# Kernel tuning notes

Hardware: AMD Instinct MI355X
Metric: run time of the kernel (lower is better)

The kernel has to match this reference:

```python
import jax, jax.numpy as jnp
import numpy as np

ALPHA = 0.5
BETA = 0.5
N_CLASS = 128
EPS = 1e-9


def setup_inputs() -> dict:
    key = jax.random.key(0)
    k1, k2 = jax.random.split(key)
    y_pred = jax.random.normal(k1, (262144, N_CLASS), dtype=jnp.float32)
    y_true = jax.random.randint(k2, (262144,), 0, N_CLASS, dtype=jnp.int64)
    return {"y_pred": y_pred, "y_true": y_true}


def reference(y_pred, y_true):
    N = y_pred.shape[0]
    # Cross-entropy (mean reduction, as nn.CrossEntropyLoss default)
    logp = jax.nn.log_softmax(y_pred, axis=1)
    ce = -jnp.mean(jnp.take_along_axis(logp, y_true[:, None], axis=1))

    # Penalty term uses detached probabilities (y_pred.detach() in torch)
    p = jax.nn.softmax(jax.lax.stop_gradient(y_pred), axis=1)
    p1 = p[:, 0]  # probability of class 0 per sample

    # num_labels: class histogram (torch loop -> vectorized scatter-add)
    num_labels = jnp.zeros((N_CLASS,), dtype=y_pred.dtype).at[y_true].add(1.0)
    # sj(j) = beta * (1 - n_j / (sum(n) - n_0)), defined for j >= 1
    s = BETA * (1.0 - num_labels / (jnp.sum(num_labels) - num_labels[0]))

    # per-sample penalty: alpha*log(p1+eps) if label==0 else s[label]*log(1-p1+eps)
    per_sample = jnp.where(
        y_true == 0,
        ALPHA * jnp.log(p1 + EPS),
        s[y_true] * jnp.log(1.0 - p1 + EPS),
    )
    penalty = jnp.sum(per_sample)
    return ce - penalty / N
```

## Files before the change

kernel.cpp:

```cpp
#include <hip/hip_runtime.h>
#include <math.h>
#include <stdint.h>

#define NCLS 128
#define NBANK 8
constexpr float ALPHA = 0.5f;
constexpr float BETA_ = 0.5f;
constexpr float EPS_ = 1e-9f;

__global__ void zero_ws(uint32_t* __restrict__ ws) {
    const int t = threadIdx.x;
    for (int i = t; i < 3088; i += 256) ws[i] = 0u;
}

__global__ __launch_bounds__(1024, 4) void loss_main(
    const float* __restrict__ y_pred,
    const int*   __restrict__ y_true,
    double* __restrict__ gLb, unsigned int* __restrict__ gcntb,
    double* __restrict__ gceb, int nrows)
{
    __shared__ float    sL[NCLS];
    __shared__ unsigned scnt[NCLS];
    __shared__ float    sce;

    const int t = threadIdx.x;
    if (t == 0) sce = 0.f;
    if (t < NCLS) { sL[t] = 0.f; scnt[t] = 0u; }
    __syncthreads();

    const int lane = t & 63;
    const int half = lane >> 5;
    const int l32  = lane & 31;
    const int wgl  = blockIdx.x * (blockDim.x >> 6) + (t >> 6);
    const int nW   = gridDim.x * (blockDim.x >> 6);
    const int nPairs = nrows >> 1;

    float ce_local = 0.f;

    int p0 = wgl * 8;
    for (; p0 + 7 < nPairs; p0 += nW * 8) {
        float4 v[8]; int lab[8];
        const float* base = y_pred + ((size_t)(p0 << 1) + half) * NCLS + (l32 << 2);
        #pragma unroll
        for (int u = 0; u < 8; ++u) {
            v[u]   = *reinterpret_cast<const float4*>(base + (size_t)(u << 1) * NCLS);
            lab[u] = y_true[((p0 + u) << 1) + half];
        }
        __builtin_amdgcn_sched_barrier(0);

        float S[8], e0[8];
        #pragma unroll
        for (int u = 0; u < 8; ++u) {
            const float ex = __expf(v[u].x), ey = __expf(v[u].y);
            const float ez = __expf(v[u].z), ew = __expf(v[u].w);
            e0[u] = ex;
            S[u]  = (ex + ey) + (ez + ew);
            if ((lab[u] >> 2) == l32) {
                const int ls = lab[u] & 3;
                ce_local += (ls == 0) ? v[u].x : (ls == 1) ? v[u].y
                          : (ls == 2) ? v[u].z : v[u].w;
            }
        }
        #pragma unroll
        for (int off = 16; off; off >>= 1) {
            #pragma unroll
            for (int u = 0; u < 8; ++u) S[u] += __shfl_xor(S[u], off);
        }
        float e0m = 1.f, Sm = 1.f; int labm = 0;
        #pragma unroll
        for (int u = 0; u < 8; ++u) {
            const float b = __shfl(e0[u], half << 5);
            if (l32 == u) { e0m = b; Sm = S[u]; labm = lab[u]; }
        }
        if (l32 < 8) {
            const float logS = __logf(Sm);
            ce_local -= logS;
            const float d = (labm == 0) ? e0m : (Sm - e0m);
            const float c0 = __logf(__fmaf_rn(EPS_, Sm, d)) - logS;
            const float contrib = (labm == 0) ? ALPHA * c0 : c0;
            atomicAdd(&sL[labm], contrib);
            atomicAdd(&scnt[labm], 1u);
        }
    }
    for (; p0 < nPairs; ++p0) {
        const int row = (p0 << 1) + half;
        const float4 v = *reinterpret_cast<const float4*>(
            y_pred + (size_t)row * NCLS + (l32 << 2));
        const int lab = y_true[row];
        const float ex = __expf(v.x), ey = __expf(v.y);
        const float ez = __expf(v.z), ew = __expf(v.w);
        float S = (ex + ey) + (ez + ew);
        if ((lab >> 2) == l32) {
            const int ls = lab & 3;
            ce_local += (ls == 0) ? v.x : (ls == 1) ? v.y : (ls == 2) ? v.z : v.w;
        }
        #pragma unroll
        for (int off = 16; off; off >>= 1) S += __shfl_xor(S, off);
        if (l32 == 0) {
            const float logS = __logf(S);
            ce_local -= logS;
            const float d = (lab == 0) ? ex : (S - ex);
            const float c0 = __logf(__fmaf_rn(EPS_, S, d)) - logS;
            const float contrib = (lab == 0) ? ALPHA * c0 : c0;
            atomicAdd(&sL[lab], contrib);
            atomicAdd(&scnt[lab], 1u);
        }
    }
    if ((nrows & 1) && wgl == 0) {
        const int row = nrows - 1;
        const float4 v = *reinterpret_cast<const float4*>(
            y_pred + (size_t)row * NCLS + (l32 << 2));
        const int lab = y_true[row];
        if (half == 0) {
            const float ex = __expf(v.x), ey = __expf(v.y);
            const float ez = __expf(v.z), ew = __expf(v.w);
            float S = (ex + ey) + (ez + ew);
            if ((lab >> 2) == l32) {
                const int ls = lab & 3;
                ce_local += (ls == 0) ? v.x : (ls == 1) ? v.y : (ls == 2) ? v.z : v.w;
            }
            #pragma unroll
            for (int off = 16; off; off >>= 1) S += __shfl_xor(S, off);
            if (l32 == 0) {
                const float logS = __logf(S);
                ce_local -= logS;
                const float d = (lab == 0) ? ex : (S - ex);
                const float c0 = __logf(__fmaf_rn(EPS_, S, d)) - logS;
                const float contrib = (lab == 0) ? ALPHA * c0 : c0;
                atomicAdd(&sL[lab], contrib);
                atomicAdd(&scnt[lab], 1u);
            }
        }
    }

    float lp = ce_local;
    #pragma unroll
    for (int off = 32; off; off >>= 1) lp += __shfl_xor(lp, off);
    if (lane == 0) atomicAdd(&sce, lp);
    __syncthreads();

    const int bank = blockIdx.x & (NBANK - 1);
    if (t < NCLS) {
        const int c = (t + blockIdx.x) & (NCLS - 1);
        if (scnt[c]) {
            atomicAdd(&gLb[c * NBANK + bank], (double)sL[c]);
            atomicAdd(&gcntb[c * NBANK + bank], scnt[c]);
        }
    }
    if (t == 0) atomicAdd(&gceb[bank], (double)sce);
}

__global__ void loss_final(const double* __restrict__ gLb,
                           const unsigned int* __restrict__ gcntb,
                           const double* __restrict__ gceb,
                           float* __restrict__ out, int nrows)
{
    const int lane = threadIdx.x;
    double cnt0 = 0.0;
    #pragma unroll
    for (int b = 0; b < NBANK; ++b) cnt0 += (double)gcntb[0 * NBANK + b];
    const double denom = (double)nrows - cnt0;

    double local = 0.0;
    for (int c = lane; c < NCLS; c += 64) {
        double Lc = 0.0, nc = 0.0;
        #pragma unroll
        for (int b = 0; b < NBANK; ++b) {
            Lc += gLb[c * NBANK + b];
            nc += (double)gcntb[c * NBANK + b];
        }
        if (c == 0) local += Lc;
        else        local += (double)BETA_ * (1.0 - nc / denom) * Lc;
    }
    #pragma unroll
    for (int off = 32; off; off >>= 1) local += __shfl_down(local, off);
    if (lane == 0) {
        double ce = 0.0;
        #pragma unroll
        for (int b = 0; b < NBANK; ++b) ce += gceb[b];
        ce = -ce / (double)nrows;
        out[0] = (float)(ce - local / (double)nrows);
    }
}

extern "C" void kernel_launch(void* const* d_in, const int* in_sizes, int n_in,
                              void* d_out, int out_size, void* d_ws, size_t ws_size,
                              hipStream_t stream) {
    const float* y_pred = (const float*)d_in[0];
    const int*   y_true = (const int*)d_in[1];
    const int nrows = in_sizes[1];

    double*   gLb   = (double*)d_ws;
    double*   gceb  = (double*)((char*)d_ws + 8192);
    unsigned* gcntb = (unsigned*)((char*)d_ws + 8256);

    zero_ws<<<dim3(1), dim3(256), 0, stream>>>((uint32_t*)d_ws);

    loss_main<<<dim3(256), dim3(1024), 0, stream>>>(y_pred, y_true, gLb, gcntb, gceb, nrows);
    loss_final<<<dim3(1), dim3(64), 0, stream>>>(gLb, gcntb, gceb, (float*)d_out, nrows);
}
```

Baseline: 38.33 us.

## Replace global atomic banks with per-block partial writes and drop zeroing kernel

Each block now writes its per-class sums, counts and CE partial to its own slot instead of issuing double/uint atomics into 8 shared banks. This removes the zero_ws kernel launch and the global atomic contention. In exchange, the single-wavefront final kernel must sum 256 partials per class, a serial loop of 256 iterations per lane over strided memory, and the workspace grows.

```diff
diff --git a/kernel.cpp b/kernel.cpp
--- a/kernel.cpp
+++ b/kernel.cpp
@@ -3,15 +3,11 @@
 #include <stdint.h>
 
 #define NCLS 128
-#define NBANK 8
+#define NBLK 256
 constexpr float ALPHA = 0.5f;
 constexpr float BETA_ = 0.5f;
 constexpr float EPS_ = 1e-9f;
 
-__global__ void zero_ws(uint32_t* __restrict__ ws) {
-    const int t = threadIdx.x;
-    for (int i = t; i < 3088; i += 256) ws[i] = 0u;
-}
 
 __global__ __launch_bounds__(1024, 4) void loss_main(
     const float* __restrict__ y_pred,
@@ -139,15 +135,11 @@
     if (lane == 0) atomicAdd(&sce, lp);
     __syncthreads();
 
-    const int bank = blockIdx.x & (NBANK - 1);
     if (t < NCLS) {
-        const int c = (t + blockIdx.x) & (NCLS - 1);
-        if (scnt[c]) {
-            atomicAdd(&gLb[c * NBANK + bank], (double)sL[c]);
-            atomicAdd(&gcntb[c * NBANK + bank], scnt[c]);
-        }
+        gLb[t * NBLK + blockIdx.x]   = (double)sL[t];
+        gcntb[t * NBLK + blockIdx.x] = scnt[t];
     }
-    if (t == 0) atomicAdd(&gceb[bank], (double)sce);
+    if (t == 0) gceb[blockIdx.x] = (double)sce;
 }
 
 __global__ void loss_final(const double* __restrict__ gLb,
@@ -156,29 +148,33 @@
                            float* __restrict__ out, int nrows)
 {
     const int lane = threadIdx.x;
+
     double cnt0 = 0.0;
+    for (int b = lane; b < NBLK; b += 64) cnt0 += (double)gcntb[b];
     #pragma unroll
-    for (int b = 0; b < NBANK; ++b) cnt0 += (double)gcntb[0 * NBANK + b];
+    for (int off = 32; off; off >>= 1) cnt0 += __shfl_xor(cnt0, off);
     const double denom = (double)nrows - cnt0;
 
     double local = 0.0;
     for (int c = lane; c < NCLS; c += 64) {
         double Lc = 0.0, nc = 0.0;
-        #pragma unroll
-        for (int b = 0; b < NBANK; ++b) {
-            Lc += gLb[c * NBANK + b];
-            nc += (double)gcntb[c * NBANK + b];
+        for (int b = 0; b < NBLK; ++b) {
+            Lc += gLb[c * NBLK + b];
+            nc += (double)gcntb[c * NBLK + b];
         }
-        if (c == 0) local += Lc;
-        else        local += (double)BETA_ * (1.0 - nc / denom) * Lc;
+        local += (c == 0) ? Lc
+               : (double)BETA_ * (1.0 - nc / denom) * Lc;
     }
+    double cep = 0.0;
+    for (int b = lane; b < NBLK; b += 64) cep += gceb[b];
+
     #pragma unroll
-    for (int off = 32; off; off >>= 1) local += __shfl_down(local, off);
+    for (int off = 32; off; off >>= 1) {
+        local += __shfl_down(local, off);
+        cep   += __shfl_down(cep, off);
+    }
     if (lane == 0) {
-        double ce = 0.0;
-        #pragma unroll
-        for (int b = 0; b < NBANK; ++b) ce += gceb[b];
-        ce = -ce / (double)nrows;
+        const double ce = -cep / (double)nrows;
         out[0] = (float)(ce - local / (double)nrows);
     }
 }
@@ -191,11 +187,9 @@
     const int nrows = in_sizes[1];
 
     double*   gLb   = (double*)d_ws;
-    double*   gceb  = (double*)((char*)d_ws + 8192);
-    unsigned* gcntb = (unsigned*)((char*)d_ws + 8256);
+    double*   gceb  = (double*)((char*)d_ws + 262144);
+    unsigned* gcntb = (unsigned*)((char*)d_ws + 264192);
 
-    zero_ws<<<dim3(1), dim3(256), 0, stream>>>((uint32_t*)d_ws);
-
-    loss_main<<<dim3(256), dim3(1024), 0, stream>>>(y_pred, y_true, gLb, gcntb, gceb, nrows);
+    loss_main<<<dim3(NBLK), dim3(1024), 0, stream>>>(y_pred, y_true, gLb, gcntb, gceb, nrows);
     loss_final<<<dim3(1), dim3(64), 0, stream>>>(gLb, gcntb, gceb, (float*)d_out, nrows);
 }
```

After: 57.62 us. +50.3%, slower.
